# Kernel tuning notes

Hardware: AMD Instinct MI355X
Metric: run time of the kernel (lower is better)

## Reference

```python
import jax, jax.numpy as jnp
import numpy as np

EPS = 1e-9
# exp factors for iterations i = 4,3,2,1,0,-1,-2 ; i == -2 -> 0.0
EXP_FACTORS = np.array([-(4.0 ** i) if i != -2 else 0.0 for i in range(4, -3, -1)], dtype=np.float32)


def setup_inputs() -> dict:
    key = jax.random.key(0)
    k1, k2 = jax.random.split(key)
    B, N, D = 16, 2048, 256
    preds = jax.random.normal(k1, (B, N, D), dtype=jnp.float32)
    labels = jax.random.normal(k2, (B, N, D), dtype=jnp.float32)
    return {"preds": preds, "labels": labels}


def _pairwise_dist(p1, p2):
    # [B,N,1] + [B,1,N] - 2 * p1 @ p2^T -> [B,N,N]
    p1_norm = jnp.sum(p1 * p1, axis=-1)[..., :, None]
    p2_norm = jnp.sum(p2 * p2, axis=-1)[..., None, :]
    return p1_norm + p2_norm - 2.0 * jnp.einsum('bnd,bmd->bnm', p1, p2)


def _approx_match(pwdist):
    B, N, _ = pwdist.shape
    match0 = jnp.zeros_like(pwdist)
    currency0 = jnp.ones((B, N, 1), dtype=pwdist.dtype)
    cost0 = jnp.ones((B, 1, N), dtype=pwdist.dtype)

    def body(carry, exp_factor):
        match, cost, currency = carry
        bids = jnp.exp(exp_factor * pwdist) * cost              # [B,N,N]
        bids = bids * currency / (jnp.sum(bids, axis=2, keepdims=True) + EPS)
        bid_wt = jnp.minimum(cost / (jnp.sum(bids, axis=1, keepdims=True) + EPS), 1.0)
        bids = bids * bid_wt
        match = match + bids
        cost = jnp.maximum(cost - jnp.sum(bids, axis=1, keepdims=True), 0.0)
        currency = jnp.maximum(currency - jnp.sum(bids, axis=2, keepdims=True), 0.0)
        return (match, cost, currency), None

    (match, _, _), _ = jax.lax.scan(body, (match0, cost0, currency0), jnp.asarray(EXP_FACTORS))
    return match


def reference(preds, labels):
    pwdist = _pairwise_dist(preds, labels)
    match = _approx_match(pwdist)
    return jnp.sum(match * pwdist)
```

## Files before the change

### kernel.cpp

```cpp
#include <hip/hip_runtime.h>
#include <cstdint>

#define B_ 16
#define N_ 2048
#define D_ 256
#define EPS_ 1e-9f

#define AS1 __attribute__((address_space(1)))
#define AS3 __attribute__((address_space(3)))

typedef float f4 __attribute__((ext_vector_type(4)));
typedef float f16v __attribute__((ext_vector_type(16)));
typedef int v8i __attribute__((ext_vector_type(8)));

__device__ float blockReduceSum(float x, float* red){
  int tid = threadIdx.x;
  red[tid] = x; __syncthreads();
  #pragma unroll
  for (int off = 128; off > 0; off >>= 1){
    if (tid < off) red[tid] += red[tid + off];
    __syncthreads();
  }
  float r = red[0]; __syncthreads();
  return r;
}

__global__ __launch_bounds__(256) void prep_kernel(
    const float* __restrict__ preds, const float* __restrict__ labels,
    unsigned char* __restrict__ pa8, unsigned char* __restrict__ pb8,
    float* __restrict__ pn, float* __restrict__ ln,
    float* __restrict__ cost, float* __restrict__ currency,
    int* __restrict__ dmin, float* __restrict__ Ppart,
    float* __restrict__ npart, float* __restrict__ out){
  int s = blockIdx.y;
  int tid = threadIdx.x;
  if (s == 0){
    int i = blockIdx.x * 256 + tid;
    if (i < B_ * N_){ cost[i] = 1.f; currency[i] = 1.f; }
    if (i < B_) dmin[i] = 0x7f7fffff;
    if (i == 0) out[0] = 0.f;
  }
  const float* src = s ? labels : preds;
  unsigned char* dst = s ? pb8 : pa8;
  float* norms = s ? ln : pn;
  int w = tid >> 6, lane = tid & 63;
  size_t row0 = (size_t)blockIdx.x * 16 + (size_t)w * 4;
  float4 v[4];
  #pragma unroll
  for (int q = 0; q < 4; q++)
    v[q] = ((const float4*)(src + (row0 + q) * D_))[lane];
  __shared__ f4 part[4][64];
  __shared__ float nred[4];
  f4 s4;
  s4[0] = v[0].x + v[1].x + v[2].x + v[3].x;
  s4[1] = v[0].y + v[1].y + v[2].y + v[3].y;
  s4[2] = v[0].z + v[1].z + v[2].z + v[3].z;
  s4[3] = v[0].w + v[1].w + v[2].w + v[3].w;
  float nsum = 0.f;
  #pragma unroll
  for (int q = 0; q < 4; q++){
    float sum = v[q].x*v[q].x + v[q].y*v[q].y + v[q].z*v[q].z + v[q].w*v[q].w;
    #pragma unroll
    for (int off = 32; off >= 1; off >>= 1) sum += __shfl_xor(sum, off);
    if (lane == 0){ norms[row0 + q] = sum; nsum += sum; }
    int pk = 0;
    pk = __builtin_amdgcn_cvt_pk_fp8_f32(v[q].x, v[q].y, pk, false);
    pk = __builtin_amdgcn_cvt_pk_fp8_f32(v[q].z, v[q].w, pk, true);
    ((unsigned int*)(dst + (row0 + q) * D_))[lane] = (unsigned int)pk;
  }
  part[w][lane] = s4;
  if (lane == 0) nred[w] = nsum;
  __syncthreads();
  if (tid < 64){
    f4 t = part[0][tid];
    #pragma unroll
    for (int q = 1; q < 4; q++){
      t[0] += part[q][tid][0]; t[1] += part[q][tid][1];
      t[2] += part[q][tid][2]; t[3] += part[q][tid][3];
    }
    *(f4*)(Ppart + ((size_t)s * 2048 + blockIdx.x) * 256 + tid * 4) = t;
  }
  if (tid == 0)
    npart[s * 2048 + blockIdx.x] = nred[0] + nred[1] + nred[2] + nred[3];
}

__global__ __launch_bounds__(512, 2) void gemm_minmax(
    const unsigned char* __restrict__ pa, const unsigned char* __restrict__ pbm,
    const float* __restrict__ pn, const float* __restrict__ ln,
    int* __restrict__ dmin)
{
  int lid = blockIdx.x;
  int xcd = lid & 7;
  int l = lid >> 3;
  int b = 2 * xcd + (l >> 4);
  int p = l & 15;
  int tn = (p & 7) * 256;
  int tmb = (p >> 3) * 1024;
  const unsigned char* A  = pa  + (size_t)b * N_ * D_;
  const unsigned char* Bm = pbm + (size_t)b * N_ * D_;
  __shared__ __align__(16) unsigned char Bs[256 * 256];
  __shared__ __align__(16) unsigned char As[2][128 * 256];
  __shared__ float minred[8];
  int tid = threadIdx.x, lane = tid & 63, w = tid >> 6;
  int wm = (w >> 2) * 64, wn = (w & 3) * 64;
  int l31 = lane & 31, half = lane >> 5;
  int rB = lane >> 4, cB = lane & 15;
  const int SC = 0x7F7F7F7F;

  #pragma unroll
  for (int q = 0; q < 8; q++){
    int R = q * 32 + w * 4;
    int r = R + rB;
    int gc = cB ^ (r & 7);
    __builtin_amdgcn_global_load_lds(
        (const AS1 unsigned int*)(const void*)&Bm[(size_t)(tn + r) * D_ + gc * 16],
        (AS3 unsigned int*)(void*)&Bs[R * 256 + lane * 16], 16, 0, 0);
  }
  #pragma unroll
  for (int q = 0; q < 4; q++){
    int R = q * 32 + w * 4;
    int r = R + rB;
    int gc = cB ^ (r & 7);
    __builtin_amdgcn_global_load_lds(
        (const AS1 unsigned int*)(const void*)&A[(size_t)(tmb + r) * D_ + gc * 16],
        (AS3 unsigned int*)(void*)&As[0][R * 256 + lane * 16], 16, 0, 0);
  }

  float lnj[2];
  #pragma unroll
  for (int j = 0; j < 2; j++)
    lnj[j] = ln[(size_t)b * N_ + tn + wn + j * 32 + l31];

  __syncthreads();

  v8i bfr[2][4];
  #pragma unroll
  for (int j = 0; j < 2; j++){
    int rb = wn + j * 32 + l31;
    #pragma unroll
    for (int kc = 0; kc < 4; kc++){
      int c0 = kc * 4 + half * 2;
      int4 lo = *(const int4*)&Bs[rb * 256 + ((c0 ^ (rb & 7)) * 16)];
      int4 hi = *(const int4*)&Bs[rb * 256 + (((c0 + 1) ^ (rb & 7)) * 16)];
      v8i t;
      t[0] = lo.x; t[1] = lo.y; t[2] = lo.z; t[3] = lo.w;
      t[4] = hi.x; t[5] = hi.y; t[6] = hi.z; t[7] = hi.w;
      bfr[j][kc] = t;
    }
  }

  float mind = 3.4e38f;
  int buf = 0;
  for (int step = 0; step < 16; step++){
    __syncthreads();
    {
      int stn = (step + 1) & 7;
      #pragma unroll
      for (int q = 0; q < 4; q++){
        int R = q * 32 + w * 4;
        int r = R + rB;
        int gc = cB ^ (r & 7);
        __builtin_amdgcn_global_load_lds(
            (const AS1 unsigned int*)(const void*)&A[(size_t)(tmb + stn * 128 + r) * D_ + gc * 16],
            (AS3 unsigned int*)(void*)&As[buf ^ 1][R * 256 + lane * 16], 16, 0, 0);
      }
    }
    f16v acc[2][2];
    #pragma unroll
    for (int i = 0; i < 2; i++)
      #pragma unroll
      for (int j = 0; j < 2; j++) acc[i][j] = (f16v)0.f;

    #pragma unroll
    for (int kc = 0; kc < 4; kc++){
      v8i af[2];
      #pragma unroll
      for (int i = 0; i < 2; i++){
        int ra = wm + i * 32 + l31;
        int c0 = kc * 4 + half * 2;
        int4 lo = *(const int4*)&As[buf][ra * 256 + ((c0 ^ (ra & 7)) * 16)];
        int4 hi = *(const int4*)&As[buf][ra * 256 + (((c0 + 1) ^ (ra & 7)) * 16)];
        v8i t;
        t[0] = lo.x; t[1] = lo.y; t[2] = lo.z; t[3] = lo.w;
        t[4] = hi.x; t[5] = hi.y; t[6] = hi.z; t[7] = hi.w;
        af[i] = t;
      }
      #pragma unroll
      for (int i = 0; i < 2; i++)
        #pragma unroll
        for (int j = 0; j < 2; j++)
          acc[i][j] = __builtin_amdgcn_mfma_scale_f32_32x32x64_f8f6f4(
              af[i], bfr[j][kc], acc[i][j], 0, 0, 0, SC, 0, SC);
    }

    int tm = tmb + (step & 7) * 128;
    #pragma unroll
    for (int i = 0; i < 2; i++){
      float4 pnq[4];
      #pragma unroll
      for (int q = 0; q < 4; q++)
        pnq[q] = *(const float4*)&pn[(size_t)b * N_ + tm + wm + i * 32 + half * 4 + q * 8];
      #pragma unroll
      for (int j = 0; j < 2; j++){
        #pragma unroll
        for (int reg = 0; reg < 16; reg++){
          float pv = ((const float*)&pnq[reg >> 2])[reg & 3];
          float v = pv + lnj[j] - 2.f * acc[i][j][reg];
          mind = fminf(mind, v);
        }
      }
    }
    buf ^= 1;
  }

  #pragma unroll
  for (int off = 32; off >= 1; off >>= 1) mind = fminf(mind, __shfl_xor(mind, off));
  if (lane == 0) minred[w] = mind;
  __syncthreads();
  if (tid == 0){
    float m = minred[0];
    #pragma unroll
    for (int q = 1; q < 8; q++) m = fminf(m, minred[q]);
    atomicMin(&dmin[b], __float_as_int(fmaxf(m, 0.f)));
  }
}

__global__ __launch_bounds__(256) void tail(
    const float* __restrict__ preds, const float* __restrict__ labels,
    const float* __restrict__ pn, const float* __restrict__ ln,
    float* __restrict__ cost, float* __restrict__ currency,
    const int* __restrict__ dmin, const float* __restrict__ Ppart,
    const float* __restrict__ npart, float* __restrict__ out)
{
  const float EF[6] = {-256.f, -64.f, -16.f, -4.f, -1.f, -0.25f};
  int b = blockIdx.x, tid = threadIdx.x;
  float dm = __int_as_float(dmin[b]);
  __shared__ float red[256];

  if (-0.25f * (dm - 16.f) < -55.f){
    float Pc = 0.f, Lc = 0.f;
    for (int k = 0; k < 128; k++){
      Pc += Ppart[((size_t)b * 128 + k) * 256 + tid];
      Lc += Ppart[((size_t)(2048 + b * 128 + k)) * 256 + tid];
    }
    float np = (tid < 128) ? npart[b * 128 + tid] : 0.f;
    float nl = (tid < 128) ? npart[2048 + b * 128 + tid] : 0.f;
    float Spn = blockReduceSum(np, red);
    float Sln = blockReduceSum(nl, red);
    float dot = blockReduceSum(Pc * Lc, red);
    if (tid == 0) atomicAdd(out, Spn + Sln - dot * (1.f / 1024.f));
    return;
  }

  __shared__ float alpha_l[N_];
  __shared__ float prow[D_];
  const float* A  = preds  + (size_t)b * N_ * D_;
  const float* Bm = labels + (size_t)b * N_ * D_;
  const float* pnb = pn + (size_t)b * N_;
  const float* lnb = ln + (size_t)b * N_;
  float* costb = cost + (size_t)b * N_;
  float* curb  = currency + (size_t)b * N_;
  for (int it = 0; it < 6; it++){
    float ef = EF[it];
    if (ef * (dm - 16.f) < -55.f) continue;
    float cost_c[8], colsum_c[8], bw_c[8], costnew_c[8];
    #pragma unroll
    for (int j = 0; j < 8; j++){ cost_c[j] = costb[j*256+tid]; colsum_c[j] = 0.f; }
    for (int r = 0; r < N_; r++){
      prow[tid] = A[(size_t)r * D_ + tid];
      __syncthreads();
      float s_c[8], rs = 0.f;
      for (int j = 0; j < 8; j++){
        int m = j*256+tid; float dot = 0.f;
        for (int k = 0; k < D_; k++) dot += prow[k] * Bm[(size_t)m * D_ + k];
        float d = pnb[r] + lnb[m] - 2.f*dot;
        float s = __expf(ef * d) * cost_c[j];
        s_c[j] = s; rs += s;
      }
      float tot = blockReduceSum(rs, red);
      float a = curb[r] / (tot + EPS_);
      if (tid == 0) alpha_l[r] = a;
      #pragma unroll
      for (int j = 0; j < 8; j++) colsum_c[j] += s_c[j] * a;
      __syncthreads();
    }
    #pragma unroll
    for (int j = 0; j < 8; j++){
      float cs = colsum_c[j];
      float bw = fminf(cost_c[j] / (cs + EPS_), 1.f);
      bw_c[j] = bw; costnew_c[j] = fmaxf(cost_c[j] - bw*cs, 0.f);
    }
    float contrib = 0.f;
    for (int r = 0; r < N_; r++){
      prow[tid] = A[(size_t)r * D_ + tid];
      __syncthreads();
      float a = alpha_l[r], rbs = 0.f;
      for (int j = 0; j < 8; j++){
        int m = j*256+tid; float dot = 0.f;
        for (int k = 0; k < D_; k++) dot += prow[k] * Bm[(size_t)m * D_ + k];
        float d = pnb[r] + lnb[m] - 2.f*dot;
        float bid = __expf(ef * d) * cost_c[j] * a * bw_c[j];
        rbs += bid; contrib += bid * d;
      }
      float tot = blockReduceSum(rbs, red);
      if (tid == 0) curb[r] = fmaxf(curb[r] - tot, 0.f);
      __syncthreads();
    }
    #pragma unroll
    for (int j = 0; j < 8; j++) costb[j*256+tid] = costnew_c[j];
    float ctot = blockReduceSum(contrib, red);
    if (tid == 0) atomicAdd(out, ctot);
    __syncthreads();
  }
  float s = 0.f;
  #pragma unroll
  for (int j = 0; j < 8; j++) s += costb[j*256+tid];
  float Sc = blockReduceSum(s, red);
  float sa = 0.f, spn = 0.f;
  #pragma unroll
  for (int j = 0; j < 8; j++){
    int i = j*256+tid;
    float a = curb[i] / (Sc + EPS_);
    alpha_l[i] = a; sa += a; spn += a * pnb[i];
  }
  float Sa  = blockReduceSum(sa, red);
  float Spn = blockReduceSum(spn, red);
  float Pc = 0.f;
  for (int r = 0; r < N_; r++)
    Pc += alpha_l[r] * A[(size_t)r * D_ + tid];
  __syncthreads();
  float sv = 0.f, sln = 0.f;
  #pragma unroll
  for (int j = 0; j < 8; j++){
    int i = j*256+tid;
    float c = costb[i];
    float bw = fminf(c / (c * Sa + EPS_), 1.f);
    float vv = c * bw;
    alpha_l[i] = vv; sv += vv; sln += vv * lnb[i];
  }
  float Sv  = blockReduceSum(sv, red);
  float Sln = blockReduceSum(sln, red);
  float Lc = 0.f;
  for (int m = 0; m < N_; m++)
    Lc += alpha_l[m] * Bm[(size_t)m * D_ + tid];
  float dot = blockReduceSum(Pc * Lc, red);
  if (tid == 0) atomicAdd(out, Spn * Sv + Sa * Sln - 2.f * dot);
}

extern "C" void kernel_launch(void* const* d_in, const int* in_sizes, int n_in,
                              void* d_out, int out_size, void* d_ws, size_t ws_size,
                              hipStream_t stream)
{
  const float* preds  = (const float*)d_in[0];
  const float* labels = (const float*)d_in[1];
  float* out = (float*)d_out;
  char* ws = (char*)d_ws;
  const size_t BN = (size_t)B_ * N_;
  size_t off = 0;
  float* cost     = (float*)(ws + off); off += BN * 4;
  float* currency = (float*)(ws + off); off += BN * 4;
  float* pn       = (float*)(ws + off); off += BN * 4;
  float* ln       = (float*)(ws + off); off += BN * 4;
  int*   dmin     = (int*)(ws + off);   off += 256;
  float* npart    = (float*)(ws + off); off += (size_t)2 * 2048 * 4;
  float* Ppart    = (float*)(ws + off); off += (size_t)2 * 2048 * 256 * 4;
  unsigned char* pa8 = (unsigned char*)(ws + off); off += BN * D_;
  unsigned char* pb8 = (unsigned char*)(ws + off); off += BN * D_;

  prep_kernel<<<dim3((unsigned)(BN / 16), 2), 256, 0, stream>>>(
      preds, labels, pa8, pb8, pn, ln, cost, currency, dmin, Ppart, npart, out);
  gemm_minmax<<<dim3(256), 512, 0, stream>>>(pa8, pb8, pn, ln, dmin);
  tail<<<dim3(B_), 256, 0, stream>>>(preds, labels, pn, ln, cost, currency, dmin,
                                     Ppart, npart, out);
}
```

Before: 142.2 us.

## Restructure min-distance GEMM into 256-row tiles with LDS-staged norms

The min-distance GEMM kernel now walks the 1024-row A range in four 256-row steps instead of sixteen 128-row steps. The old schedule revisited each 128-row tile twice; the new one visits each row once. Pred norms are staged in shared memory with async loads, the epilogue for one sub-tile is interleaved with the MFMAs of the next, and the B tile's LDS region is reused as the second A buffer. Shared memory use rises to about 132KB per block and the accumulators per thread double, which adds register pressure.

Result: faster. 125.4 us, median of 2 (-11.8%).

```diff
diff --git a/kernel.cpp b/kernel.cpp
--- a/kernel.cpp
+++ b/kernel.cpp
@@ -98,11 +98,14 @@
   int tmb = (p >> 3) * 1024;
   const unsigned char* A  = pa  + (size_t)b * N_ * D_;
   const unsigned char* Bm = pbm + (size_t)b * N_ * D_;
-  __shared__ __align__(16) unsigned char Bs[256 * 256];
-  __shared__ __align__(16) unsigned char As[2][128 * 256];
+  __shared__ __align__(16) unsigned char smem[135168];
   __shared__ float minred[8];
+  unsigned char* Bs   = smem;
+  unsigned char* bufA = smem + 65536;
+  unsigned char* bufB = smem;
+  float* pnL = (float*)(smem + 131072);
   int tid = threadIdx.x, lane = tid & 63, w = tid >> 6;
-  int wm = (w >> 2) * 64, wn = (w & 3) * 64;
+  int wm2 = (w >> 2) * 128, wn = (w & 3) * 64;
   int l31 = lane & 31, half = lane >> 5;
   int rB = lane >> 4, cB = lane & 15;
   const int SC = 0x7F7F7F7F;
@@ -115,15 +118,15 @@
     __builtin_amdgcn_global_load_lds(
         (const AS1 unsigned int*)(const void*)&Bm[(size_t)(tn + r) * D_ + gc * 16],
         (AS3 unsigned int*)(void*)&Bs[R * 256 + lane * 16], 16, 0, 0);
-  }
-  #pragma unroll
-  for (int q = 0; q < 4; q++){
-    int R = q * 32 + w * 4;
-    int r = R + rB;
-    int gc = cB ^ (r & 7);
     __builtin_amdgcn_global_load_lds(
         (const AS1 unsigned int*)(const void*)&A[(size_t)(tmb + r) * D_ + gc * 16],
-        (AS3 unsigned int*)(void*)&As[0][R * 256 + lane * 16], 16, 0, 0);
+        (AS3 unsigned int*)(void*)&bufA[R * 256 + lane * 16], 16, 0, 0);
+  }
+  #pragma unroll
+  for (int q = 0; q < 2; q++){
+    __builtin_amdgcn_global_load_lds(
+        (const AS1 unsigned int*)(const void*)&pn[(size_t)b * N_ + tmb + q * 512 + tid],
+        (AS3 unsigned int*)(void*)&pnL[q * 512 + w * 64], 4, 0, 0);
   }
 
   float lnj[2];
@@ -150,67 +153,85 @@
   }
 
   float mind = 3.4e38f;
-  int buf = 0;
-  for (int step = 0; step < 16; step++){
+  for (int t = 0; t < 4; t++){
     __syncthreads();
-    {
-      int stn = (step + 1) & 7;
-      #pragma unroll
-      for (int q = 0; q < 4; q++){
+    const unsigned char* Acur = (t & 1) ? bufB : bufA;
+    unsigned char* Anxt = (t & 1) ? bufA : bufB;
+    if (t < 3){
+      #pragma unroll
+      for (int q = 0; q < 8; q++){
         int R = q * 32 + w * 4;
         int r = R + rB;
         int gc = cB ^ (r & 7);
         __builtin_amdgcn_global_load_lds(
-            (const AS1 unsigned int*)(const void*)&A[(size_t)(tmb + stn * 128 + r) * D_ + gc * 16],
-            (AS3 unsigned int*)(void*)&As[buf ^ 1][R * 256 + lane * 16], 16, 0, 0);
-      }
-    }
-    f16v acc[2][2];
-    #pragma unroll
-    for (int i = 0; i < 2; i++)
-      #pragma unroll
-      for (int j = 0; j < 2; j++) acc[i][j] = (f16v)0.f;
-
-    #pragma unroll
-    for (int kc = 0; kc < 4; kc++){
-      v8i af[2];
-      #pragma unroll
-      for (int i = 0; i < 2; i++){
-        int ra = wm + i * 32 + l31;
+            (const AS1 unsigned int*)(const void*)&A[(size_t)(tmb + (t + 1) * 256 + r) * D_ + gc * 16],
+            (AS3 unsigned int*)(void*)&Anxt[R * 256 + lane * 16], 16, 0, 0);
+      }
+    }
+
+    f16v acc[4][2];
+    #pragma unroll
+    for (int i = 0; i < 4; i++){ acc[i][0] = (f16v)0.f; acc[i][1] = (f16v)0.f; }
+
+    int pbase = t * 256 + wm2;
+    #pragma unroll
+    for (int i = 0; i < 4; i++){
+      int ra = wm2 + i * 32 + l31;
+      v8i af[4];
+      #pragma unroll
+      for (int kc = 0; kc < 4; kc++){
         int c0 = kc * 4 + half * 2;
-        int4 lo = *(const int4*)&As[buf][ra * 256 + ((c0 ^ (ra & 7)) * 16)];
-        int4 hi = *(const int4*)&As[buf][ra * 256 + (((c0 + 1) ^ (ra & 7)) * 16)];
-        v8i t;
-        t[0] = lo.x; t[1] = lo.y; t[2] = lo.z; t[3] = lo.w;
-        t[4] = hi.x; t[5] = hi.y; t[6] = hi.z; t[7] = hi.w;
-        af[i] = t;
-      }
-      #pragma unroll
-      for (int i = 0; i < 2; i++)
+        int4 lo = *(const int4*)&Acur[ra * 256 + ((c0 ^ (ra & 7)) * 16)];
+        int4 hi = *(const int4*)&Acur[ra * 256 + (((c0 + 1) ^ (ra & 7)) * 16)];
+        v8i tt;
+        tt[0] = lo.x; tt[1] = lo.y; tt[2] = lo.z; tt[3] = lo.w;
+        tt[4] = hi.x; tt[5] = hi.y; tt[6] = hi.z; tt[7] = hi.w;
+        af[kc] = tt;
+      }
+      #pragma unroll
+      for (int kc = 0; kc < 4; kc++){
+        acc[i][0] = __builtin_amdgcn_mfma_scale_f32_32x32x64_f8f6f4(
+            af[kc], bfr[0][kc], acc[i][0], 0, 0, 0, SC, 0, SC);
+        acc[i][1] = __builtin_amdgcn_mfma_scale_f32_32x32x64_f8f6f4(
+            af[kc], bfr[1][kc], acc[i][1], 0, 0, 0, SC, 0, SC);
+      }
+      if (i > 0){
+        int ip = i - 1;
+        float4 pnq[4];
         #pragma unroll
-        for (int j = 0; j < 2; j++)
-          acc[i][j] = __builtin_amdgcn_mfma_scale_f32_32x32x64_f8f6f4(
-              af[i], bfr[j][kc], acc[i][j], 0, 0, 0, SC, 0, SC);
-    }
-
-    int tm = tmb + (step & 7) * 128;
-    #pragma unroll
-    for (int i = 0; i < 2; i++){
+        for (int q = 0; q < 4; q++)
+          pnq[q] = *(const float4*)&pnL[pbase + ip * 32 + half * 4 + q * 8];
+        #pragma unroll
+        for (int j = 0; j < 2; j++){
+          #pragma unroll
+          for (int reg = 0; reg < 16; reg += 2){
+            float pl0 = ((const float*)&pnq[reg >> 2])[reg & 3] + lnj[j];
+            float pl1 = ((const float*)&pnq[reg >> 2])[(reg & 3) + 1] + lnj[j];
+            float v0 = fmaf(-2.f, acc[ip][j][reg], pl0);
+            float v1 = fmaf(-2.f, acc[ip][j][reg + 1], pl1);
+            mind = fminf(mind, fminf(v0, v1));
+          }
+        }
+      }
+    }
+    {
+      int ip = 3;
       float4 pnq[4];
       #pragma unroll
       for (int q = 0; q < 4; q++)
-        pnq[q] = *(const float4*)&pn[(size_t)b * N_ + tm + wm + i * 32 + half * 4 + q * 8];
+        pnq[q] = *(const float4*)&pnL[pbase + ip * 32 + half * 4 + q * 8];
       #pragma unroll
       for (int j = 0; j < 2; j++){
         #pragma unroll
-        for (int reg = 0; reg < 16; reg++){
-          float pv = ((const float*)&pnq[reg >> 2])[reg & 3];
-          float v = pv + lnj[j] - 2.f * acc[i][j][reg];
-          mind = fminf(mind, v);
+        for (int reg = 0; reg < 16; reg += 2){
+          float pl0 = ((const float*)&pnq[reg >> 2])[reg & 3] + lnj[j];
+          float pl1 = ((const float*)&pnq[reg >> 2])[(reg & 3) + 1] + lnj[j];
+          float v0 = fmaf(-2.f, acc[ip][j][reg], pl0);
+          float v1 = fmaf(-2.f, acc[ip][j][reg + 1], pl1);
+          mind = fminf(mind, fminf(v0, v1));
         }
       }
     }
-    buf ^= 1;
   }
 
   #pragma unroll
```
